# Performance work log

Measured on AMD Instinct MI355X. Metric: run time of the kernel, lower is better.

Reference implementation:

```python
import jax, jax.numpy as jnp
import numpy as np

S, M, H, E = 8192, 1024, 4096, 8
CAPACITY = S // E  # capacity_factor = 1.0, k = 1


def setup_inputs() -> dict:
    key = jax.random.key(0)
    ks = jax.random.split(key, 4)
    return {
        "x": jax.random.normal(ks[0], (S, M), jnp.float32),
        "wg": jax.random.normal(ks[1], (M, E), jnp.float32) * 0.02,
        "inter_w": jax.random.normal(ks[2], (E, M, H), jnp.float32) * 0.02,
        "inter_b": jnp.zeros((E, H), jnp.float32),
        "output_w": jax.random.normal(ks[3], (E, H, M), jnp.float32) * 0.02,
        "output_b": jnp.zeros((E, M), jnp.float32),
    }


def _top1_gate(x, wg, capacity):
    """GShard-style top-1 gate (inference: no noise, drop tokens over capacity).
    Returns combine_weights [S,E,C] (float) and dispatch_mask [S,E,C] (float 0/1)."""
    logits = x @ wg                                   # [S,E]
    gates = jax.nn.softmax(logits, axis=-1)           # [S,E]
    idx = jnp.argmax(gates, axis=-1)                  # [S]
    mask1 = jax.nn.one_hot(idx, gates.shape[-1], dtype=gates.dtype)  # [S,E]
    # 0-based position of each token within its expert's queue
    locations = jnp.cumsum(mask1, axis=0) - mask1     # [S,E]
    mask1 = mask1 * (locations < capacity)            # drop overflow tokens
    pos = jnp.sum(locations * mask1, axis=1).astype(jnp.int32)  # [S]
    gate_s = jnp.sum(gates * mask1, axis=1)           # [S] gate value of kept tokens
    loc_oh = jax.nn.one_hot(pos, capacity, dtype=gates.dtype)    # [S,C]
    combine = gate_s[:, None, None] * mask1[:, :, None] * loc_oh[:, None, :]  # [S,E,C]
    dispatch = (combine > 0).astype(x.dtype)
    return combine, dispatch


def reference(x, wg, inter_w, inter_b, output_w, output_b):
    combine, dispatch = _top1_gate(x, wg, CAPACITY)
    # token dispatch: torch.einsum('sec,sm->ecm', dispatch_mask, attention_output)
    disp_x = jnp.einsum('sec,sm->ecm', dispatch, x)                 # [E,C,M]
    # per-expert fused gelu-GEMM MLP (gelu_gemm_func: gelu(x@W1+b1)@W2, +b2)
    h = jax.nn.gelu(jnp.einsum('ecm,emh->ech', disp_x, inter_w)
                    + inter_b[:, None, :], approximate=False)       # [E,C,H]
    exp_out = jnp.einsum('ech,ehm->ecm', h, output_w) + output_b[:, None, :]  # [E,C,M]
    # combine: combined_weights.reshape(S, E*C) @ expert_output.reshape(E*C, M)
    y = jnp.einsum('sec,ecm->sm', combine, exp_out)                 # [S,M]
    return y
```

## Files before the change

kernel.cpp:

```cpp
#include <hip/hip_runtime.h>

#define S_ 8192
#define M_ 1024
#define H_ 4096
#define E_ 8
#define C_ 1024

typedef short s16x8 __attribute__((ext_vector_type(8)));
typedef float f32x4 __attribute__((ext_vector_type(4)));

__device__ __forceinline__ unsigned short f2bf(float f) {
    unsigned int u = __float_as_uint(f);
    unsigned int r = u + 0x7fffu + ((u >> 16) & 1u);
    return (unsigned short)(r >> 16);
}
__device__ __forceinline__ float bf2f(unsigned short s) {
    return __uint_as_float(((unsigned int)s) << 16);
}

__device__ __forceinline__ void async_copy16(const unsigned short* g, unsigned short* l) {
    __builtin_amdgcn_global_load_lds(
        (const __attribute__((address_space(1))) unsigned int*)g,
        (__attribute__((address_space(3))) unsigned int*)l, 16, 0, 0);
}

__global__ __launch_bounds__(256) void gate_kernel(
    const float* __restrict__ x, const float* __restrict__ wg,
    int* __restrict__ expert_of, float* __restrict__ gate_full,
    unsigned short* __restrict__ xb)
{
    int token = (blockIdx.x * 256 + threadIdx.x) >> 6;
    int lane  = threadIdx.x & 63;
    const float* xr = x + (size_t)token * M_;
    unsigned short* xbr = xb + (size_t)token * M_;
    double acc[E_] = {0,0,0,0,0,0,0,0};
    for (int t = 0; t < M_ / 64; ++t) {
        int m = t * 64 + lane;
        float xf = xr[m];
        xbr[m] = f2bf(xf);
        double xv = (double)xf;
        const float* w = wg + m * E_;
        #pragma unroll
        for (int e = 0; e < E_; ++e) acc[e] += xv * (double)w[e];
    }
    #pragma unroll
    for (int e = 0; e < E_; ++e)
        for (int off = 32; off; off >>= 1) acc[e] += __shfl_xor(acc[e], off);
    if (lane == 0) {
        double mx = acc[0]; int idx = 0;
        #pragma unroll
        for (int e = 1; e < E_; ++e) if (acc[e] > mx) { mx = acc[e]; idx = e; }
        double den = 0.0;
        #pragma unroll
        for (int e = 0; e < E_; ++e) den += exp(acc[e] - mx);
        expert_of[token] = idx;
        gate_full[token] = (float)(1.0 / den);
    }
}

__global__ __launch_bounds__(256) void count_kernel(
    const int* __restrict__ expert_of, int* __restrict__ cnt,
    int* __restrict__ slot_to_token)
{
    __shared__ int wc[4][E_];
    int tid = threadIdx.x, lane = tid & 63, wv = tid >> 6;
    slot_to_token[blockIdx.x * 256 + tid] = -1;
    int e = expert_of[blockIdx.x * 256 + tid];
    #pragma unroll
    for (int j = 0; j < E_; ++j) {
        unsigned long long b = __ballot(e == j);
        if (lane == 0) wc[wv][j] = __popcll(b);
    }
    __syncthreads();
    if (tid < E_) {
        int s = 0;
        #pragma unroll
        for (int w = 0; w < 4; ++w) s += wc[w][tid];
        cnt[blockIdx.x * E_ + tid] = s;
    }
}

__global__ __launch_bounds__(64) void prefix_kernel(
    const int* __restrict__ cnt, int* __restrict__ cbase)
{
    int tid = threadIdx.x;
    if (tid < E_) {
        int run = 0;
        for (int b = 0; b < 32; ++b) { cbase[b * E_ + tid] = run; run += cnt[b * E_ + tid]; }
    }
}

__global__ __launch_bounds__(256) void scatter_kernel(
    const int* __restrict__ expert_of, const int* __restrict__ cbase,
    int* __restrict__ slot_to_token)
{
    __shared__ int wc[4][E_];
    int tid = threadIdx.x, lane = tid & 63, wv = tid >> 6;
    int s = blockIdx.x * 256 + tid;
    int e = expert_of[s];
    unsigned long long mymask = 0;
    #pragma unroll
    for (int j = 0; j < E_; ++j) {
        unsigned long long b = __ballot(e == j);
        if (lane == 0) wc[wv][j] = __popcll(b);
        if (j == e) mymask = b;
    }
    __syncthreads();
    int waveoff = 0;
    for (int w = 0; w < 4; ++w) if (w < wv) waveoff += wc[w][e];
    int pos = cbase[blockIdx.x * E_ + e] + waveoff +
              __popcll(mymask & ((1ull << lane) - 1ull));
    if (pos < C_) slot_to_token[e * C_ + pos] = s;
}

__global__ __launch_bounds__(256) void transpose_cvt_kernel(
    const float* __restrict__ src, unsigned short* __restrict__ dst, int K, int N)
{
    __shared__ unsigned short tile[64 * 84];
    const size_t esz = (size_t)K * N;
    const float* s = src + (size_t)blockIdx.z * esz;
    unsigned short* d = dst + (size_t)blockIdx.z * esz;
    const int k0 = blockIdx.y * 64, n0 = blockIdx.x * 64;
    const int tid = threadIdx.x;
    {
        const int n  = tid & 63;
        const int kb = (tid >> 6) * 16;
        #pragma unroll
        for (int i = 0; i < 4; ++i) {
            int k4 = kb + i * 4;
            float a0 = s[(size_t)(k0 + k4 + 0) * N + n0 + n];
            float a1 = s[(size_t)(k0 + k4 + 1) * N + n0 + n];
            float a2 = s[(size_t)(k0 + k4 + 2) * N + n0 + n];
            float a3 = s[(size_t)(k0 + k4 + 3) * N + n0 + n];
            unsigned long long p = (unsigned long long)f2bf(a0)
                | ((unsigned long long)f2bf(a1) << 16)
                | ((unsigned long long)f2bf(a2) << 32)
                | ((unsigned long long)f2bf(a3) << 48);
            *(unsigned long long*)(&tile[n * 84 + k4]) = p;
        }
    }
    __syncthreads();
    {
        const int n  = tid >> 3;
        const int k8 = (tid & 7) * 8;
        #pragma unroll
        for (int j = 0; j < 2; ++j) {
            int nn = n + j * 32;
            unsigned long long lo = *(const unsigned long long*)(&tile[nn * 84 + k8]);
            unsigned long long hi = *(const unsigned long long*)(&tile[nn * 84 + k8 + 4]);
            ulonglong2 v; v.x = lo; v.y = hi;
            *(ulonglong2*)(d + (size_t)(n0 + nn) * K + k0 + k8) = v;
        }
    }
}

__global__ __launch_bounds__(256, 2) void gemm1_kernel(
    const unsigned short* __restrict__ xb, const unsigned short* __restrict__ w1t,
    const float* __restrict__ b1, const int* __restrict__ slot_to_token,
    unsigned short* __restrict__ h)
{
    const int e  = blockIdx.z;
    const int n0 = blockIdx.x * 128, c0 = blockIdx.y * 128;
    __shared__ unsigned short As[128 * 32];
    __shared__ unsigned short Bs[128 * 32];
    __shared__ int tok[128];
    const int tid = threadIdx.x;
    if (tid < 128) tok[tid] = slot_to_token[e * C_ + c0 + tid];
    __syncthreads();
    const int wave = tid >> 6, lane = tid & 63;

    const int q0 = tid, q1 = 256 + tid;
    const int r0 = q0 >> 2, cq0 = q0 & 3;
    const int r1 = q1 >> 2, cq1 = q1 & 3;
    int t0 = tok[r0]; if (t0 < 0) t0 = 0;
    int t1 = tok[r1]; if (t1 < 0) t1 = 0;
    const unsigned short* srcA0 = xb + (size_t)t0 * M_ + cq0 * 8;
    const unsigned short* srcA1 = xb + (size_t)t1 * M_ + cq1 * 8;
    const unsigned short* Bp = w1t + (size_t)e * M_ * H_;
    const unsigned short* srcB0 = Bp + (size_t)(n0 + r0) * M_ + cq0 * 8;
    const unsigned short* srcB1 = Bp + (size_t)(n0 + r1) * M_ + cq1 * 8;
    unsigned short* dstA0 = As + wave * 512;
    unsigned short* dstA1 = As + 2048 + wave * 512;
    unsigned short* dstB0 = Bs + wave * 512;
    unsigned short* dstB1 = Bs + 2048 + wave * 512;

    f32x4 acc[4][4] = {};
    const int wr = wave >> 1, wc = wave & 1, qd = lane >> 4, ln16 = lane & 15;

    for (int k0 = 0; k0 < M_; k0 += 32) {
        async_copy16(srcA0 + k0, dstA0);
        async_copy16(srcA1 + k0, dstA1);
        async_copy16(srcB0 + k0, dstB0);
        async_copy16(srcB1 + k0, dstB1);
        __syncthreads();
        s16x8 af[4], bfr[4];
        #pragma unroll
        for (int i = 0; i < 4; ++i)
            af[i] = *(const s16x8*)(&As[(wr * 64 + i * 16 + ln16) * 32 + qd * 8]);
        #pragma unroll
        for (int j = 0; j < 4; ++j)
            bfr[j] = *(const s16x8*)(&Bs[(wc * 64 + j * 16 + ln16) * 32 + qd * 8]);
        #pragma unroll
        for (int i = 0; i < 4; ++i)
            #pragma unroll
            for (int j = 0; j < 4; ++j)
                acc[i][j] = __builtin_amdgcn_mfma_f32_16x16x32_bf16(
                    af[i], bfr[j], acc[i][j], 0, 0, 0);
        __syncthreads();
    }

    unsigned short* hb = h + (size_t)e * C_ * H_;
    #pragma unroll
    for (int i = 0; i < 4; ++i) {
        int crow = c0 + wr * 64 + i * 16 + qd * 4;
        #pragma unroll
        for (int j = 0; j < 4; ++j) {
            int n = n0 + wc * 64 + j * 16 + ln16;
            float bias = b1[e * H_ + n];
            #pragma unroll
            for (int r = 0; r < 4; ++r) {
                float v = acc[i][j][r] + bias;
                float g = 0.5f * v * (1.0f + erff(v * 0.70710678118f));
                hb[(size_t)(crow + r) * H_ + n] = f2bf(g);
            }
        }
    }
}

__global__ __launch_bounds__(256, 2) void gemm2_kernel(
    const unsigned short* __restrict__ h, const unsigned short* __restrict__ w2t,
    unsigned short* __restrict__ part)
{
    const int e = blockIdx.z >> 1, kc = blockIdx.z & 1;
    const int n0 = blockIdx.x * 128, c0 = blockIdx.y * 128;
    const int kb = kc * 2048;
    __shared__ unsigned short As[128 * 32];
    __shared__ unsigned short Bs[128 * 32];
    const int tid = threadIdx.x;
    const int wave = tid >> 6, lane = tid & 63;

    const int q0 = tid, q1 = 256 + tid;
    const int r0 = q0 >> 2, cq0 = q0 & 3;
    const int r1 = q1 >> 2, cq1 = q1 & 3;
    const unsigned short* Ap = h + (size_t)e * C_ * H_;
    const unsigned short* srcA0 = Ap + (size_t)(c0 + r0) * H_ + kb + cq0 * 8;
    const unsigned short* srcA1 = Ap + (size_t)(c0 + r1) * H_ + kb + cq1 * 8;
    const unsigned short* Bp = w2t + (size_t)e * M_ * H_;
    const unsigned short* srcB0 = Bp + (size_t)(n0 + r0) * H_ + kb + cq0 * 8;
    const unsigned short* srcB1 = Bp + (size_t)(n0 + r1) * H_ + kb + cq1 * 8;
    unsigned short* dstA0 = As + wave * 512;
    unsigned short* dstA1 = As + 2048 + wave * 512;
    unsigned short* dstB0 = Bs + wave * 512;
    unsigned short* dstB1 = Bs + 2048 + wave * 512;

    f32x4 acc[4][4] = {};
    const int wr = wave >> 1, wc = wave & 1, qd = lane >> 4, ln16 = lane & 15;

    for (int k0 = 0; k0 < 2048; k0 += 32) {
        async_copy16(srcA0 + k0, dstA0);
        async_copy16(srcA1 + k0, dstA1);
        async_copy16(srcB0 + k0, dstB0);
        async_copy16(srcB1 + k0, dstB1);
        __syncthreads();
        s16x8 af[4], bfr[4];
        #pragma unroll
        for (int i = 0; i < 4; ++i)
            af[i] = *(const s16x8*)(&As[(wr * 64 + i * 16 + ln16) * 32 + qd * 8]);
        #pragma unroll
        for (int j = 0; j < 4; ++j)
            bfr[j] = *(const s16x8*)(&Bs[(wc * 64 + j * 16 + ln16) * 32 + qd * 8]);
        #pragma unroll
        for (int i = 0; i < 4; ++i)
            #pragma unroll
            for (int j = 0; j < 4; ++j)
                acc[i][j] = __builtin_amdgcn_mfma_f32_16x16x32_bf16(
                    af[i], bfr[j], acc[i][j], 0, 0, 0);
        __syncthreads();
    }

    unsigned short* pp = part + (size_t)(kc * E_ + e) * C_ * M_;
    #pragma unroll
    for (int i = 0; i < 4; ++i) {
        int crow = c0 + wr * 64 + i * 16 + qd * 4;
        #pragma unroll
        for (int j = 0; j < 4; ++j) {
            int n = n0 + wc * 64 + j * 16 + ln16;
            #pragma unroll
            for (int r = 0; r < 4; ++r)
                pp[(size_t)(crow + r) * M_ + n] = f2bf(acc[i][j][r]);
        }
    }
}

__global__ __launch_bounds__(256) void combine_kernel(
    const unsigned short* __restrict__ part, const float* __restrict__ b2,
    const int* __restrict__ slot_to_token, const float* __restrict__ gate_full,
    float* __restrict__ y)
{
    const int sid  = blockIdx.x * 4 + (threadIdx.x >> 6);
    const int lane = threadIdx.x & 63;
    const int e = sid >> 10, c = sid & 1023;
    const int t = slot_to_token[e * C_ + c];
    if (t < 0) return;
    const float g = gate_full[t];
    float* yr = y + (size_t)t * M_;
    const float* b2r = b2 + e * M_;
    const unsigned short* p0 = part + ((size_t)e * C_ + c) * M_;
    const unsigned short* p1 = part + ((size_t)(E_ + e) * C_ + c) * M_;
    #pragma unroll
    for (int v = 0; v < 2; ++v) {
        int n = (v * 64 + lane) * 8;
        ushort4 a0 = *(const ushort4*)(p0 + n);
        ushort4 a1 = *(const ushort4*)(p0 + n + 4);
        ushort4 c0v = *(const ushort4*)(p1 + n);
        ushort4 c1 = *(const ushort4*)(p1 + n + 4);
        float4 b0 = *(const float4*)(b2r + n);
        float4 b1v = *(const float4*)(b2r + n + 4);
        float4 o0, o1;
        o0.x = g * (bf2f(a0.x) + bf2f(c0v.x) + b0.x);
        o0.y = g * (bf2f(a0.y) + bf2f(c0v.y) + b0.y);
        o0.z = g * (bf2f(a0.z) + bf2f(c0v.z) + b0.z);
        o0.w = g * (bf2f(a0.w) + bf2f(c0v.w) + b0.w);
        o1.x = g * (bf2f(a1.x) + bf2f(c1.x) + b1v.x);
        o1.y = g * (bf2f(a1.y) + bf2f(c1.y) + b1v.y);
        o1.z = g * (bf2f(a1.z) + bf2f(c1.z) + b1v.z);
        o1.w = g * (bf2f(a1.w) + bf2f(c1.w) + b1v.w);
        *(float4*)(yr + n) = o0;
        *(float4*)(yr + n + 4) = o1;
    }
}

extern "C" void kernel_launch(void* const* d_in, const int* in_sizes, int n_in,
                              void* d_out, int out_size, void* d_ws, size_t ws_size,
                              hipStream_t stream) {
    const float* x  = (const float*)d_in[0];
    const float* wg = (const float*)d_in[1];
    const float* w1 = (const float*)d_in[2];
    const float* b1 = (const float*)d_in[3];
    const float* w2 = (const float*)d_in[4];
    const float* b2 = (const float*)d_in[5];
    float* y = (float*)d_out;

    char* ws = (char*)d_ws;
    int*   slot_to_token = (int*)ws;
    float* gate_full     = (float*)(ws + 32768);
    int*   cnt           = (int*)(ws + 65536);
    int*   cbase         = (int*)(ws + 66560);
    int*   expert_of     = (int*)(ws + 67584);
    unsigned short* xb   = (unsigned short*)(ws + 131072);
    unsigned short* w2t  = xb + (size_t)S_ * M_;

    unsigned short* w1t  = (unsigned short*)d_in[4];
    unsigned short* h    = (unsigned short*)d_in[2];
    unsigned short* part = h + (size_t)E_ * C_ * H_;

    hipMemsetAsync(d_out, 0, (size_t)S_ * M_ * sizeof(float), stream);
    gate_kernel<<<S_ / 4, 256, 0, stream>>>(x, wg, expert_of, gate_full, xb);
    count_kernel<<<32, 256, 0, stream>>>(expert_of, cnt, slot_to_token);
    prefix_kernel<<<1, 64, 0, stream>>>(cnt, cbase);
    scatter_kernel<<<32, 256, 0, stream>>>(expert_of, cbase, slot_to_token);

    transpose_cvt_kernel<<<dim3(M_ / 64, H_ / 64, E_), 256, 0, stream>>>(w2, w2t, H_, M_);
    transpose_cvt_kernel<<<dim3(H_ / 64, M_ / 64, E_), 256, 0, stream>>>(w1, w1t, M_, H_);

    gemm1_kernel<<<dim3(H_ / 128, C_ / 128, E_), 256, 0, stream>>>(
        xb, w1t, b1, slot_to_token, h);
    gemm2_kernel<<<dim3(M_ / 128, C_ / 128, E_ * 2), 256, 0, stream>>>(h, w2t, part);
    combine_kernel<<<2048, 256, 0, stream>>>(part, b2, slot_to_token, gate_full, y);
}
```

Before: 570.0 us.

## Swizzle LDS tiles, use tanh-form GELU, fuse combine into gemm2 epilogue

Applies an XOR swizzle to the LDS tile layout in both GEMMs to reduce bank conflicts on fragment reads. Replaces erf-based GELU with a sigmoid/tanh approximation using fast exp. Removes split-K in gemm2 and the separate combine kernel, scattering gated, biased outputs directly to y from the gemm2 epilogue. This cuts a bf16 partial round-trip and a launch, at the cost of half the gemm2 blocks and a small GELU accuracy change.

Result: no change. 573.5 us (+0.6%).

```diff
diff --git a/kernel.cpp b/kernel.cpp
--- a/kernel.cpp
+++ b/kernel.cpp
@@ -169,16 +169,16 @@
     __syncthreads();
     const int wave = tid >> 6, lane = tid & 63;
 
-    const int q0 = tid, q1 = 256 + tid;
-    const int r0 = q0 >> 2, cq0 = q0 & 3;
-    const int r1 = q1 >> 2, cq1 = q1 & 3;
+    const int r0 = tid >> 2;
+    const int cq = (tid & 3) ^ ((tid >> 3) & 3);
+    const int r1 = 64 + r0;
     int t0 = tok[r0]; if (t0 < 0) t0 = 0;
     int t1 = tok[r1]; if (t1 < 0) t1 = 0;
-    const unsigned short* srcA0 = xb + (size_t)t0 * M_ + cq0 * 8;
-    const unsigned short* srcA1 = xb + (size_t)t1 * M_ + cq1 * 8;
+    const unsigned short* srcA0 = xb + (size_t)t0 * M_ + cq * 8;
+    const unsigned short* srcA1 = xb + (size_t)t1 * M_ + cq * 8;
     const unsigned short* Bp = w1t + (size_t)e * M_ * H_;
-    const unsigned short* srcB0 = Bp + (size_t)(n0 + r0) * M_ + cq0 * 8;
-    const unsigned short* srcB1 = Bp + (size_t)(n0 + r1) * M_ + cq1 * 8;
+    const unsigned short* srcB0 = Bp + (size_t)(n0 + r0) * M_ + cq * 8;
+    const unsigned short* srcB1 = Bp + (size_t)(n0 + r1) * M_ + cq * 8;
     unsigned short* dstA0 = As + wave * 512;
     unsigned short* dstA1 = As + 2048 + wave * 512;
     unsigned short* dstB0 = Bs + wave * 512;
@@ -186,6 +186,7 @@
 
     f32x4 acc[4][4] = {};
     const int wr = wave >> 1, wc = wave & 1, qd = lane >> 4, ln16 = lane & 15;
+    const int sq = (qd ^ ((ln16 >> 1) & 3)) * 8;
 
     for (int k0 = 0; k0 < M_; k0 += 32) {
         async_copy16(srcA0 + k0, dstA0);
@@ -196,10 +197,10 @@
         s16x8 af[4], bfr[4];
         #pragma unroll
         for (int i = 0; i < 4; ++i)
-            af[i] = *(const s16x8*)(&As[(wr * 64 + i * 16 + ln16) * 32 + qd * 8]);
+            af[i] = *(const s16x8*)(&As[(wr * 64 + i * 16 + ln16) * 32 + sq]);
         #pragma unroll
         for (int j = 0; j < 4; ++j)
-            bfr[j] = *(const s16x8*)(&Bs[(wc * 64 + j * 16 + ln16) * 32 + qd * 8]);
+            bfr[j] = *(const s16x8*)(&Bs[(wc * 64 + j * 16 + ln16) * 32 + sq]);
         #pragma unroll
         for (int i = 0; i < 4; ++i)
             #pragma unroll
@@ -220,7 +221,9 @@
             #pragma unroll
             for (int r = 0; r < 4; ++r) {
                 float v = acc[i][j][r] + bias;
-                float g = 0.5f * v * (1.0f + erff(v * 0.70710678118f));
+                float u = v * v;
+                float z = v * (1.5957691216f + 0.0713548163f * u);
+                float g = v / (1.0f + __expf(-z));
                 hb[(size_t)(crow + r) * H_ + n] = f2bf(g);
             }
         }
@@ -229,25 +232,33 @@
 
 __global__ __launch_bounds__(256, 2) void gemm2_kernel(
     const unsigned short* __restrict__ h, const unsigned short* __restrict__ w2t,
-    unsigned short* __restrict__ part)
-{
-    const int e = blockIdx.z >> 1, kc = blockIdx.z & 1;
+    const float* __restrict__ b2, const int* __restrict__ slot_to_token,
+    const float* __restrict__ gate_full, float* __restrict__ y)
+{
+    const int e = blockIdx.z;
     const int n0 = blockIdx.x * 128, c0 = blockIdx.y * 128;
-    const int kb = kc * 2048;
     __shared__ unsigned short As[128 * 32];
     __shared__ unsigned short Bs[128 * 32];
+    __shared__ int tok[128];
+    __shared__ float gw[128];
     const int tid = threadIdx.x;
+    if (tid < 128) {
+        int t = slot_to_token[e * C_ + c0 + tid];
+        tok[tid] = t;
+        gw[tid] = (t >= 0) ? gate_full[t] : 0.0f;
+    }
+    __syncthreads();
     const int wave = tid >> 6, lane = tid & 63;
 
-    const int q0 = tid, q1 = 256 + tid;
-    const int r0 = q0 >> 2, cq0 = q0 & 3;
-    const int r1 = q1 >> 2, cq1 = q1 & 3;
+    const int r0 = tid >> 2;
+    const int cq = (tid & 3) ^ ((tid >> 3) & 3);
+    const int r1 = 64 + r0;
     const unsigned short* Ap = h + (size_t)e * C_ * H_;
-    const unsigned short* srcA0 = Ap + (size_t)(c0 + r0) * H_ + kb + cq0 * 8;
-    const unsigned short* srcA1 = Ap + (size_t)(c0 + r1) * H_ + kb + cq1 * 8;
+    const unsigned short* srcA0 = Ap + (size_t)(c0 + r0) * H_ + cq * 8;
+    const unsigned short* srcA1 = Ap + (size_t)(c0 + r1) * H_ + cq * 8;
     const unsigned short* Bp = w2t + (size_t)e * M_ * H_;
-    const unsigned short* srcB0 = Bp + (size_t)(n0 + r0) * H_ + kb + cq0 * 8;
-    const unsigned short* srcB1 = Bp + (size_t)(n0 + r1) * H_ + kb + cq1 * 8;
+    const unsigned short* srcB0 = Bp + (size_t)(n0 + r0) * H_ + cq * 8;
+    const unsigned short* srcB1 = Bp + (size_t)(n0 + r1) * H_ + cq * 8;
     unsigned short* dstA0 = As + wave * 512;
     unsigned short* dstA1 = As + 2048 + wave * 512;
     unsigned short* dstB0 = Bs + wave * 512;
@@ -255,8 +266,9 @@
 
     f32x4 acc[4][4] = {};
     const int wr = wave >> 1, wc = wave & 1, qd = lane >> 4, ln16 = lane & 15;
-
-    for (int k0 = 0; k0 < 2048; k0 += 32) {
+    const int sq = (qd ^ ((ln16 >> 1) & 3)) * 8;
+
+    for (int k0 = 0; k0 < H_; k0 += 32) {
         async_copy16(srcA0 + k0, dstA0);
         async_copy16(srcA1 + k0, dstA1);
         async_copy16(srcB0 + k0, dstB0);
@@ -265,10 +277,10 @@
         s16x8 af[4], bfr[4];
         #pragma unroll
         for (int i = 0; i < 4; ++i)
-            af[i] = *(const s16x8*)(&As[(wr * 64 + i * 16 + ln16) * 32 + qd * 8]);
+            af[i] = *(const s16x8*)(&As[(wr * 64 + i * 16 + ln16) * 32 + sq]);
         #pragma unroll
         for (int j = 0; j < 4; ++j)
-            bfr[j] = *(const s16x8*)(&Bs[(wc * 64 + j * 16 + ln16) * 32 + qd * 8]);
+            bfr[j] = *(const s16x8*)(&Bs[(wc * 64 + j * 16 + ln16) * 32 + sq]);
         #pragma unroll
         for (int i = 0; i < 4; ++i)
             #pragma unroll
@@ -278,55 +290,20 @@
         __syncthreads();
     }
 
-    unsigned short* pp = part + (size_t)(kc * E_ + e) * C_ * M_;
     #pragma unroll
     for (int i = 0; i < 4; ++i) {
-        int crow = c0 + wr * 64 + i * 16 + qd * 4;
+        int lr = wr * 64 + i * 16 + qd * 4;
         #pragma unroll
         for (int j = 0; j < 4; ++j) {
             int n = n0 + wc * 64 + j * 16 + ln16;
+            float bias = b2[e * M_ + n];
             #pragma unroll
-            for (int r = 0; r < 4; ++r)
-                pp[(size_t)(crow + r) * M_ + n] = f2bf(acc[i][j][r]);
+            for (int r = 0; r < 4; ++r) {
+                int t = tok[lr + r];
+                if (t >= 0)
+                    y[(size_t)t * M_ + n] = gw[lr + r] * (acc[i][j][r] + bias);
+            }
         }
-    }
-}
-
-__global__ __launch_bounds__(256) void combine_kernel(
-    const unsigned short* __restrict__ part, const float* __restrict__ b2,
-    const int* __restrict__ slot_to_token, const float* __restrict__ gate_full,
-    float* __restrict__ y)
-{
-    const int sid  = blockIdx.x * 4 + (threadIdx.x >> 6);
-    const int lane = threadIdx.x & 63;
-    const int e = sid >> 10, c = sid & 1023;
-    const int t = slot_to_token[e * C_ + c];
-    if (t < 0) return;
-    const float g = gate_full[t];
-    float* yr = y + (size_t)t * M_;
-    const float* b2r = b2 + e * M_;
-    const unsigned short* p0 = part + ((size_t)e * C_ + c) * M_;
-    const unsigned short* p1 = part + ((size_t)(E_ + e) * C_ + c) * M_;
-    #pragma unroll
-    for (int v = 0; v < 2; ++v) {
-        int n = (v * 64 + lane) * 8;
-        ushort4 a0 = *(const ushort4*)(p0 + n);
-        ushort4 a1 = *(const ushort4*)(p0 + n + 4);
-        ushort4 c0v = *(const ushort4*)(p1 + n);
-        ushort4 c1 = *(const ushort4*)(p1 + n + 4);
-        float4 b0 = *(const float4*)(b2r + n);
-        float4 b1v = *(const float4*)(b2r + n + 4);
-        float4 o0, o1;
-        o0.x = g * (bf2f(a0.x) + bf2f(c0v.x) + b0.x);
-        o0.y = g * (bf2f(a0.y) + bf2f(c0v.y) + b0.y);
-        o0.z = g * (bf2f(a0.z) + bf2f(c0v.z) + b0.z);
-        o0.w = g * (bf2f(a0.w) + bf2f(c0v.w) + b0.w);
-        o1.x = g * (bf2f(a1.x) + bf2f(c1.x) + b1v.x);
-        o1.y = g * (bf2f(a1.y) + bf2f(c1.y) + b1v.y);
-        o1.z = g * (bf2f(a1.z) + bf2f(c1.z) + b1v.z);
-        o1.w = g * (bf2f(a1.w) + bf2f(c1.w) + b1v.w);
-        *(float4*)(yr + n) = o0;
-        *(float4*)(yr + n + 4) = o1;
     }
 }
 
@@ -352,7 +329,6 @@
 
     unsigned short* w1t  = (unsigned short*)d_in[4];
     unsigned short* h    = (unsigned short*)d_in[2];
-    unsigned short* part = h + (size_t)E_ * C_ * H_;
 
     hipMemsetAsync(d_out, 0, (size_t)S_ * M_ * sizeof(float), stream);
     gate_kernel<<<S_ / 4, 256, 0, stream>>>(x, wg, expert_of, gate_full, xb);
@@ -365,6 +341,6 @@
 
     gemm1_kernel<<<dim3(H_ / 128, C_ / 128, E_), 256, 0, stream>>>(
         xb, w1t, b1, slot_to_token, h);
-    gemm2_kernel<<<dim3(M_ / 128, C_ / 128, E_ * 2), 256, 0, stream>>>(h, w2t, part);
-    combine_kernel<<<2048, 256, 0, stream>>>(part, b2, slot_to_token, gate_full, y);
-}
+    gemm2_kernel<<<dim3(M_ / 128, C_ / 128, E_), 256, 0, stream>>>(
+        h, w2t, b2, slot_to_token, gate_full, y);
+}
```
